# Performance work log

Hardware: AMD Instinct MI355X
Metric: run time of the kernel (lower is better)

Reference implementation:

```python
import jax, jax.numpy as jnp
import numpy as np
import math

B, DK, DV, T, H, W = 4, 64, 512, 2, 64, 64


def setup_inputs() -> dict:
    key = jax.random.key(0)
    k1, k2, k3, k4 = jax.random.split(key, 4)
    qkey = jax.random.normal(k1, (B, DK, H, W), dtype=jnp.float32)
    qval = jax.random.normal(k2, (B, DV, H, W), dtype=jnp.float32)
    mkey = jax.random.normal(k3, (B, DK, T, H, W), dtype=jnp.float32)
    mval = jax.random.normal(k4, (B, DV, T, H, W), dtype=jnp.float32)
    qmask = jnp.ones((B, 1, H, W), dtype=bool)
    mmask = jnp.ones((B, 1, T, H, W), dtype=bool)
    return {"qkey": qkey, "qval": qval, "qmask": qmask,
            "mkey": mkey, "mval": mval, "mmask": mmask}


def reference(qkey, qval, qmask, mkey, mval, mmask):
    # maskRead: masked cross-attention from query pixels to memory pixels.
    b, dk, h, w = qkey.shape
    dv = qval.shape[1]
    t = mkey.shape[2]
    n = h * w            # query positions
    m = t * h * w        # memory positions
    qk = qkey.reshape(b, dk, n)
    mk = mkey.reshape(b, dk, m)
    mv = mval.reshape(b, dv, m)
    qm = qmask.reshape(b, n)
    mm = mmask.reshape(b, m)
    scale = np.float32(1.0 / math.sqrt(dk))
    # scores[b, m, n] = mk^T @ qk  (softmax over memory axis m, as in torch dim=0)
    scores = jnp.einsum('bdm,bdn->bmn', mk, qk) * scale
    neg = jnp.asarray(-1e30, scores.dtype)
    scores = jnp.where(mm[:, :, None], scores, neg)
    p = jax.nn.softmax(scores, axis=1)  # [b, m, n]
    read = jnp.einsum('bvm,bmn->bvn', mv, p)  # [b, dv, n]
    # write only at masked query positions; elsewhere qread stays zero
    qread = jnp.where(qm[:, None, :], read, jnp.zeros_like(read))
    return qread.reshape(b, dv, h, w)
```

## Files before the change

### kernel.cpp

```cpp
#include <hip/hip_runtime.h>
#include <hip/hip_bf16.h>


#define NB 4
#define DKC 64
#define DVC 512
#define NQ 4096
#define NKV 8192
#define KB 64
#define NT2 128
#define DVG 128
#define NWG 512

typedef float f32x4 __attribute__((ext_vector_type(4)));
typedef float f32x16 __attribute__((ext_vector_type(16)));
typedef short s16x8 __attribute__((ext_vector_type(8)));
typedef unsigned short u16;
typedef unsigned int u32;
typedef u32 u32x4 __attribute__((ext_vector_type(4)));
typedef u16 u16x8 __attribute__((ext_vector_type(8)));
typedef u16 u16x4 __attribute__((ext_vector_type(4)));

__device__ __forceinline__ u16 f2bf_rne(float f) {
  union { float f; unsigned u; } v; v.f = f;
  return (u16)((v.u + 0x7FFFu + ((v.u >> 16) & 1u)) >> 16);
}

template <int SWZ>
__global__ __launch_bounds__(256) void transpose_bf16_64(
    const float* __restrict__ src, u16* __restrict__ dst, int M, float scale) {
  __shared__ float tt[64][65];
  const int tid = threadIdx.x;
  const int b = blockIdx.y;
  const int m0 = blockIdx.x * 64;
  {
    const int mi = tid & 63;
    const int dr = (tid >> 6) * 16;
    const float* s = src + ((size_t)b * 64 + dr) * M + m0 + mi;
#pragma unroll
    for (int j = 0; j < 16; ++j) tt[dr + j][mi] = s[(size_t)j * M];
  }
  __syncthreads();
  {
    const int mo = tid >> 2;
    const int d0 = (tid & 3) * 16;
    const int X = SWZ ? ((mo & 7) << 3) : 0;
    u16x8 o0, o1;
#pragma unroll
    for (int j = 0; j < 8; ++j) {
      o0[j] = f2bf_rne(tt[d0 + j][mo] * scale);
      o1[j] = f2bf_rne(tt[d0 + 8 + j][mo] * scale);
    }
    u16* base = dst + (size_t)b * M * 64 + (size_t)blockIdx.x * 4096 + mo * 64;
    *(u16x8*)(base + (d0 ^ X)) = o0;
    *(u16x8*)(base + ((d0 + 8) ^ X)) = o1;
  }
}

__global__ __launch_bounds__(256) void conv_v_tiles(const float* __restrict__ src,
                                                    u16* __restrict__ dst) {
  const size_t i = ((size_t)blockIdx.x * 256 + threadIdx.x) * 8;
  const int m = (int)(i & (NKV - 1));
  const size_t bd = i >> 13;
  const int dv = (int)(bd & (DVC - 1));
  const int b = (int)(bd >> 9);
  const float4 a = *(const float4*)(src + i);
  const float4 c = *(const float4*)(src + i + 4);
  u16x8 o;
  o[0] = f2bf_rne(a.x); o[1] = f2bf_rne(a.y); o[2] = f2bf_rne(a.z); o[3] = f2bf_rne(a.w);
  o[4] = f2bf_rne(c.x); o[5] = f2bf_rne(c.y); o[6] = f2bf_rne(c.z); o[7] = f2bf_rne(c.w);
  const int combo = b * 4 + (dv >> 7);
  const int row = dv & 127;
  const size_t off = (size_t)combo * (128 * 128 * 64) + (size_t)(m >> 6) * (128 * 64) +
                     row * 64 + ((m & 63) ^ ((row & 7) << 3));
  *(u16x8*)(dst + off) = o;
}

#define GLL(GP, LP)                                                            \
  __builtin_amdgcn_global_load_lds(                                            \
      (const __attribute__((address_space(1))) void*)(GP),                     \
      (__attribute__((address_space(3))) void*)(LP), 16, 0, 0)

#define PACK_QUARTER(SV, H, DST)                                               \
  {                                                                            \
    const float e0 = exp2f((SV)[(H) * 8 + 0]), e1 = exp2f((SV)[(H) * 8 + 1]);  \
    const float e2 = exp2f((SV)[(H) * 8 + 2]), e3 = exp2f((SV)[(H) * 8 + 3]);  \
    const float e4 = exp2f((SV)[(H) * 8 + 4]), e5 = exp2f((SV)[(H) * 8 + 5]);  \
    const float e6 = exp2f((SV)[(H) * 8 + 6]), e7 = exp2f((SV)[(H) * 8 + 7]);  \
    lacc += ((e0 + e1) + (e2 + e3)) + ((e4 + e5) + (e6 + e7));                 \
    u32 a0_, a1_, a2_, a3_;                                                    \
    asm("v_cvt_pk_bf16_f32 %0, %1, %2" : "=v"(a0_) : "v"(e0), "v"(e1));        \
    asm("v_cvt_pk_bf16_f32 %0, %1, %2" : "=v"(a1_) : "v"(e2), "v"(e3));        \
    asm("v_cvt_pk_bf16_f32 %0, %1, %2" : "=v"(a2_) : "v"(e4), "v"(e5));        \
    asm("v_cvt_pk_bf16_f32 %0, %1, %2" : "=v"(a3_) : "v"(e6), "v"(e7));        \
    asm("v_permlane32_swap_b32 %0, %1" : "+v"(a0_), "+v"(a2_));                \
    asm("v_permlane32_swap_b32 %0, %1" : "+v"(a1_), "+v"(a3_));                \
    union { u32x4 u; s16x8 s; } cv_;                                           \
    cv_.u[0] = a0_; cv_.u[1] = a1_; cv_.u[2] = a2_; cv_.u[3] = a3_;            \
    (DST) = cv_.s;                                                             \
  }

__global__ __launch_bounds__(256, 2) void maskread_main(
    const u16* __restrict__ kT, const u16* __restrict__ qT,
    const u16* __restrict__ vb, float* __restrict__ outp) {
  __shared__ __align__(16) u16 Vlds[2][DVG * KB];

  const int tid = threadIdx.x;
  const int w = tid >> 6;
  const int lane = tid & 63;
  const int l31 = lane & 31;
  const int hi = lane >> 5;

  const int logical = (blockIdx.x & 7) * (NWG / 8) + (blockIdx.x >> 3);
  const int combo = logical >> 5;
  const int qt = logical & 31;
  const int b = combo >> 2;
  const int g = combo & 3;
  const int nq = qt * 128 + w * 32 + l31;

  const u16* qp = qT + ((size_t)b * NQ + nq) * DKC + hi * 8;
  s16x8 qf[4];
#pragma unroll
  for (int ks = 0; ks < 4; ++ks) qf[ks] = *(const s16x8*)(qp + ks * 16);

  const int sw8 = (l31 & 7) << 3;
  int roff[4];
#pragma unroll
  for (int ks = 0; ks < 4; ++ks) roff[ks] = l31 * 64 + ((ks * 16 + hi * 8) ^ sw8);

  const u16* kgb = kT + (size_t)b * (128 * 4096);
  const u16* vgb = vb + (size_t)combo * (128 * 8192);

  f32x16 oacc[4];
#pragma unroll
  for (int dvt = 0; dvt < 4; ++dvt)
#pragma unroll
    for (int rr = 0; rr < 16; ++rr) oacc[dvt][rr] = 0.f;
  float lacc = 0.f;

  s16x8 ka[2][4];
#pragma unroll
  for (int kvt = 0; kvt < 2; ++kvt)
#pragma unroll
    for (int ks = 0; ks < 4; ++ks)
      ka[kvt][ks] = *(const s16x8*)(kgb + kvt * 2048 + roff[ks]);
  {
    const u16* vp0 = vgb + w * 2048 + lane * 8;
#pragma unroll
    for (int j = 0; j < 4; ++j) GLL(vp0 + j * 512, &Vlds[0][w * 2048 + j * 512]);
  }
  __syncthreads();

  for (int t = 0; t < NT2; ++t) {
    const int cur = t & 1;
    if (t + 1 < NT2) {
      const u16* vp_ = vgb + (size_t)(t + 1) * 8192 + w * 2048 + lane * 8;
#pragma unroll
      for (int j = 0; j < 4; ++j) GLL(vp_ + j * 512, &Vlds[cur ^ 1][w * 2048 + j * 512]);
    }

    f32x16 sacc[2];
#pragma unroll
    for (int kvt = 0; kvt < 2; ++kvt) {
#pragma unroll
      for (int rr = 0; rr < 16; ++rr) sacc[kvt][rr] = 0.f;
#pragma unroll
      for (int ks = 0; ks < 4; ++ks)
        sacc[kvt] = __builtin_amdgcn_mfma_f32_32x32x16_bf16(ka[kvt][ks], qf[ks], sacc[kvt], 0, 0, 0);
    }

    if (t + 1 < NT2) {
      const u16* kp_ = kgb + (size_t)(t + 1) * 4096;
#pragma unroll
      for (int kvt = 0; kvt < 2; ++kvt)
#pragma unroll
        for (int ks = 0; ks < 4; ++ks)
          ka[kvt][ks] = *(const s16x8*)(kp_ + kvt * 2048 + roff[ks]);
    }

    const u16* Vl = &Vlds[cur][0];
    __builtin_amdgcn_s_setprio(1);
    s16x8 pf[4];
#pragma unroll
    for (int ks = 0; ks < 4; ++ks) {
      PACK_QUARTER(sacc[ks >> 1], ks & 1, pf[ks]);
#pragma unroll
      for (int dvt = 0; dvt < 4; ++dvt) {
        const s16x8 va = *(const s16x8*)&Vl[roff[ks] + dvt * 2048];
        oacc[dvt] = __builtin_amdgcn_mfma_f32_32x32x16_bf16(va, pf[ks], oacc[dvt], 0, 0, 0);
      }
    }
    __builtin_amdgcn_s_setprio(0);

    __syncthreads();
  }

  const float lt = lacc + __shfl_xor(lacc, 32);
  const float rinv = 1.f / lt;
  float* ob = outp + ((size_t)(b * DVC + g * DVG)) * NQ + nq;
#pragma unroll
  for (int dvt = 0; dvt < 4; ++dvt)
#pragma unroll
    for (int rr = 0; rr < 16; ++rr) {
      const int dv = dvt * 32 + (rr & 3) + 8 * (rr >> 2) + 4 * hi;
      ob[(size_t)dv * NQ] = oacc[dvt][rr] * rinv;
    }
}

__global__ __launch_bounds__(512, 2) void maskread_attn_fb(
    const float* __restrict__ qkey, const float* __restrict__ mkey,
    const float* __restrict__ mval, float* __restrict__ out) {
  __shared__ __align__(16) u16 Qlds[64 * DKC];
  __shared__ __align__(16) u16 Klds1[128 * DKC];
  __shared__ __align__(16) u16 Plds1[64 * 128];
  __shared__ float psum_lds[8][64];

  const int tid = threadIdx.x;
  const int w = tid >> 6;
  const int l15 = tid & 15;
  const int lhi = (tid & 63) >> 4;
  const int logical = (blockIdx.x & 7) * 32 + (blockIdx.x >> 3);
  const int b = logical >> 6;
  const int n0 = (logical & 63) * 64;
  const float C2 = 0.18033688011112042f;

  {
    const int d = tid >> 3;
    const int q8 = (tid & 7) * 8;
    const float* src = qkey + ((b * DKC + d) * NQ) + n0 + q8;
    const float4 v0 = *(const float4*)(src);
    const float4 v1 = *(const float4*)(src + 4);
    const float vv[8] = {v0.x, v0.y, v0.z, v0.w, v1.x, v1.y, v1.z, v1.w};
#pragma unroll
    for (int j = 0; j < 8; ++j) {
      const int q = q8 + j;
      Qlds[q * DKC + (d ^ ((q & 7) << 3))] = f2bf_rne(vv[j]);
    }
  }

  f32x4 oacc[4][4];
#pragma unroll
  for (int mt = 0; mt < 4; ++mt)
#pragma unroll
    for (int nt = 0; nt < 4; ++nt)
#pragma unroll
      for (int i = 0; i < 4; ++i) oacc[mt][nt][i] = 0.f;
  float lacc[4] = {0.f, 0.f, 0.f, 0.f};

  const int dvb = w * 64;
  for (int kt = 0; kt < 64; ++kt) {
    const int kv0 = kt * 128;
    {
      const int d = tid >> 3;
      const int k16 = (tid & 7) * 16;
      const float* src = mkey + ((b * DKC + d) * NKV) + kv0 + k16;
#pragma unroll
      for (int i = 0; i < 4; ++i) {
        const float4 v = *(const float4*)(src + i * 4);
        const float vv4[4] = {v.x * C2, v.y * C2, v.z * C2, v.w * C2};
#pragma unroll
        for (int j = 0; j < 4; ++j) {
          const int k = k16 + i * 4 + j;
          Klds1[k * DKC + (d ^ ((k & 7) << 3))] = f2bf_rne(vv4[j]);
        }
      }
    }
    __syncthreads();
    f32x4 sacc[4];
#pragma unroll
    for (int nt = 0; nt < 4; ++nt)
#pragma unroll
      for (int i = 0; i < 4; ++i) sacc[nt][i] = 0.f;
#pragma unroll
    for (int ks = 0; ks < 2; ++ks) {
      const int kr = w * 16 + l15;
      const int c = ks * 32 + lhi * 8;
      const s16x8 afr = *(const s16x8*)&Klds1[kr * DKC + (c ^ ((kr & 7) << 3))];
#pragma unroll
      for (int nt = 0; nt < 4; ++nt) {
        const int q = nt * 16 + l15;
        const s16x8 bfr = *(const s16x8*)&Qlds[q * DKC + (c ^ ((q & 7) << 3))];
        sacc[nt] = __builtin_amdgcn_mfma_f32_16x16x32_bf16(afr, bfr, sacc[nt], 0, 0, 0);
      }
    }
#pragma unroll
    for (int nt = 0; nt < 4; ++nt) {
      const int q = nt * 16 + l15;
      const float p0 = exp2f(sacc[nt][0]);
      const float p1 = exp2f(sacc[nt][1]);
      const float p2 = exp2f(sacc[nt][2]);
      const float p3 = exp2f(sacc[nt][3]);
      lacc[nt] += (p0 + p1) + (p2 + p3);
      u16x4 pk;
      pk[0] = f2bf_rne(p0); pk[1] = f2bf_rne(p1); pk[2] = f2bf_rne(p2); pk[3] = f2bf_rne(p3);
      const int kvb = w * 16 + lhi * 4;
      *(u16x4*)&Plds1[q * 128 + (kvb ^ ((q & 7) << 3))] = pk;
    }
    __syncthreads();
#pragma unroll
    for (int ks = 0; ks < 4; ++ks) {
      s16x8 bfr[4];
#pragma unroll
      for (int nt = 0; nt < 4; ++nt) {
        const int q = nt * 16 + l15;
        const int kvb = ks * 32 + lhi * 8;
        bfr[nt] = *(const s16x8*)&Plds1[q * 128 + (kvb ^ ((q & 7) << 3))];
      }
#pragma unroll
      for (int mt = 0; mt < 4; ++mt) {
        const int vv = dvb + mt * 16 + l15;
        const float* src = mval + ((size_t)(b * DVC + vv) * NKV) + kv0 + ks * 32 + lhi * 8;
        const float4 a0 = *(const float4*)src;
        const float4 a1 = *(const float4*)(src + 4);
        s16x8 afr;
        afr[0] = (short)f2bf_rne(a0.x); afr[1] = (short)f2bf_rne(a0.y);
        afr[2] = (short)f2bf_rne(a0.z); afr[3] = (short)f2bf_rne(a0.w);
        afr[4] = (short)f2bf_rne(a1.x); afr[5] = (short)f2bf_rne(a1.y);
        afr[6] = (short)f2bf_rne(a1.z); afr[7] = (short)f2bf_rne(a1.w);
#pragma unroll
        for (int nt = 0; nt < 4; ++nt)
          oacc[mt][nt] = __builtin_amdgcn_mfma_f32_16x16x32_bf16(afr, bfr[nt], oacc[mt][nt], 0, 0, 0);
      }
    }
    __syncthreads();
  }
#pragma unroll
  for (int nt = 0; nt < 4; ++nt) {
    float l = lacc[nt];
    l += __shfl_xor(l, 16);
    l += __shfl_xor(l, 32);
    if (lhi == 0) psum_lds[w][nt * 16 + l15] = l;
  }
  __syncthreads();
  float linv[4];
#pragma unroll
  for (int nt = 0; nt < 4; ++nt) {
    const int q = nt * 16 + l15;
    float s = psum_lds[0][q];
#pragma unroll
    for (int ww = 1; ww < 8; ++ww) s += psum_lds[ww][q];
    linv[nt] = 1.f / s;
  }
#pragma unroll
  for (int mt = 0; mt < 4; ++mt) {
#pragma unroll
    for (int nt = 0; nt < 4; ++nt) {
      const int q = nt * 16 + l15;
#pragma unroll
      for (int i = 0; i < 4; ++i) {
        const int vv = dvb + mt * 16 + lhi * 4 + i;
        out[((size_t)(b * DVC + vv) * NQ) + n0 + q] = oacc[mt][nt][i] * linv[nt];
      }
    }
  }
}

extern "C" void kernel_launch(void* const* d_in, const int* in_sizes, int n_in,
                              void* d_out, int out_size, void* d_ws, size_t ws_size,
                              hipStream_t stream) {
  (void)in_sizes; (void)n_in; (void)out_size;
  const float* qkey = (const float*)d_in[0];
  const float* mkey = (const float*)d_in[3];
  const float* mval = (const float*)d_in[4];
  float* out = (float*)d_out;

  u16* kTp = (u16*)d_ws;
  u16* qTp = kTp + (size_t)NB * NKV * DKC;
  u16* vbp = qTp + (size_t)NB * NQ * DKC;
  const size_t need_base =
      ((size_t)NB * NKV * DKC + (size_t)NB * NQ * DKC + (size_t)NB * DVC * NKV) * 2;
  const float C2 = 0.18033688011112042f;

  if (ws_size >= need_base) {
    transpose_bf16_64<1><<<dim3(NKV / 64, NB), 256, 0, stream>>>(mkey, kTp, NKV, C2);
    transpose_bf16_64<0><<<dim3(NQ / 64, NB), 256, 0, stream>>>(qkey, qTp, NQ, 1.0f);
    conv_v_tiles<<<dim3((NB * DVC * NKV) / (256 * 8)), 256, 0, stream>>>(mval, vbp);
    maskread_main<<<dim3(NWG), dim3(256), 0, stream>>>(kTp, qTp, vbp, out);
  } else {
    maskread_attn_fb<<<dim3(256), dim3(512), 0, stream>>>(qkey, mkey, mval, out);
  }
}
```

Before: 281.7 us.

## Split KV loop across two wave groups per block with LDS reduction

Result: slower. 1.096 ms (+288.9%).

```diff
diff --git a/kernel.cpp b/kernel.cpp
--- a/kernel.cpp
+++ b/kernel.cpp
@@ -8,7 +8,6 @@
 #define NQ 4096
 #define NKV 8192
 #define KB 64
-#define NT2 128
 #define DVG 128
 #define NWG 512
 
@@ -100,23 +99,26 @@
     (DST) = cv_.s;                                                             \
   }
 
-__global__ __launch_bounds__(256, 2) void maskread_main(
+__global__ __launch_bounds__(512, 4) void maskread_main(
     const u16* __restrict__ kT, const u16* __restrict__ qT,
     const u16* __restrict__ vb, float* __restrict__ outp) {
-  __shared__ __align__(16) u16 Vlds[2][DVG * KB];
+  __shared__ __align__(16) unsigned char smem[69632];
 
   const int tid = threadIdx.x;
-  const int w = tid >> 6;
+  const int w4 = tid >> 6;
+  const int r = w4 >> 2;
+  const int wq = w4 & 3;
   const int lane = tid & 63;
   const int l31 = lane & 31;
   const int hi = lane >> 5;
+  const int t255 = tid & 255;
 
   const int logical = (blockIdx.x & 7) * (NWG / 8) + (blockIdx.x >> 3);
   const int combo = logical >> 5;
   const int qt = logical & 31;
   const int b = combo >> 2;
   const int g = combo & 3;
-  const int nq = qt * 128 + w * 32 + l31;
+  const int nq = qt * 128 + wq * 32 + l31;
 
   const u16* qp = qT + ((size_t)b * NQ + nq) * DKC + hi * 8;
   s16x8 qf[4];
@@ -128,8 +130,9 @@
 #pragma unroll
   for (int ks = 0; ks < 4; ++ks) roff[ks] = l31 * 64 + ((ks * 16 + hi * 8) ^ sw8);
 
-  const u16* kgb = kT + (size_t)b * (128 * 4096);
-  const u16* vgb = vb + (size_t)combo * (128 * 8192);
+  const u16* kgb = kT + (size_t)b * (128 * 4096) + (size_t)r * 64 * 4096;
+  const u16* vgb = vb + (size_t)combo * (128 * 8192) + (size_t)r * 64 * 8192;
+  u16* Vbase = (u16*)smem + r * 16384;
 
   f32x16 oacc[4];
 #pragma unroll
@@ -145,18 +148,19 @@
     for (int ks = 0; ks < 4; ++ks)
       ka[kvt][ks] = *(const s16x8*)(kgb + kvt * 2048 + roff[ks]);
   {
-    const u16* vp0 = vgb + w * 2048 + lane * 8;
-#pragma unroll
-    for (int j = 0; j < 4; ++j) GLL(vp0 + j * 512, &Vlds[0][w * 2048 + j * 512]);
+    const u16* vp0 = vgb + wq * 2048 + lane * 8;
+#pragma unroll
+    for (int j = 0; j < 4; ++j) GLL(vp0 + j * 512, Vbase + wq * 2048 + j * 512);
   }
   __syncthreads();
 
-  for (int t = 0; t < NT2; ++t) {
+  for (int t = 0; t < 64; ++t) {
     const int cur = t & 1;
-    if (t + 1 < NT2) {
-      const u16* vp_ = vgb + (size_t)(t + 1) * 8192 + w * 2048 + lane * 8;
-#pragma unroll
-      for (int j = 0; j < 4; ++j) GLL(vp_ + j * 512, &Vlds[cur ^ 1][w * 2048 + j * 512]);
+    if (t + 1 < 64) {
+      const u16* vp_ = vgb + (size_t)(t + 1) * 8192 + wq * 2048 + lane * 8;
+      u16* vd_ = Vbase + (cur ^ 1) * 8192 + wq * 2048;
+#pragma unroll
+      for (int j = 0; j < 4; ++j) GLL(vp_ + j * 512, vd_ + j * 512);
     }
 
     f32x16 sacc[2];
@@ -169,7 +173,7 @@
         sacc[kvt] = __builtin_amdgcn_mfma_f32_32x32x16_bf16(ka[kvt][ks], qf[ks], sacc[kvt], 0, 0, 0);
     }
 
-    if (t + 1 < NT2) {
+    if (t + 1 < 64) {
       const u16* kp_ = kgb + (size_t)(t + 1) * 4096;
 #pragma unroll
       for (int kvt = 0; kvt < 2; ++kvt)
@@ -178,16 +182,16 @@
           ka[kvt][ks] = *(const s16x8*)(kp_ + kvt * 2048 + roff[ks]);
     }
 
-    const u16* Vl = &Vlds[cur][0];
+    const u16* Vl = Vbase + cur * 8192;
     __builtin_amdgcn_s_setprio(1);
-    s16x8 pf[4];
 #pragma unroll
     for (int ks = 0; ks < 4; ++ks) {
-      PACK_QUARTER(sacc[ks >> 1], ks & 1, pf[ks]);
+      s16x8 pf;
+      PACK_QUARTER(sacc[ks >> 1], ks & 1, pf);
 #pragma unroll
       for (int dvt = 0; dvt < 4; ++dvt) {
         const s16x8 va = *(const s16x8*)&Vl[roff[ks] + dvt * 2048];
-        oacc[dvt] = __builtin_amdgcn_mfma_f32_32x32x16_bf16(va, pf[ks], oacc[dvt], 0, 0, 0);
+        oacc[dvt] = __builtin_amdgcn_mfma_f32_32x32x16_bf16(va, pf, oacc[dvt], 0, 0, 0);
       }
     }
     __builtin_amdgcn_s_setprio(0);
@@ -195,16 +199,44 @@
     __syncthreads();
   }
 
-  const float lt = lacc + __shfl_xor(lacc, 32);
+  const float ltr = lacc + __shfl_xor(lacc, 32);
+  float* redL = (float*)(smem + 67584);
+  redL[r * 256 + t255] = ltr;
+  float* X = (float*)smem;
+  if (r == 1) {
+#pragma unroll
+    for (int dvt = 0; dvt < 2; ++dvt)
+#pragma unroll
+      for (int rr = 0; rr < 16; ++rr) X[t255 * 33 + dvt * 16 + rr] = oacc[dvt][rr];
+  } else {
+#pragma unroll
+    for (int dvt = 0; dvt < 2; ++dvt)
+#pragma unroll
+      for (int rr = 0; rr < 16; ++rr) X[8448 + t255 * 33 + dvt * 16 + rr] = oacc[dvt + 2][rr];
+  }
+  __syncthreads();
+  const float lt = redL[t255] + redL[256 + t255];
   const float rinv = 1.f / lt;
   float* ob = outp + ((size_t)(b * DVC + g * DVG)) * NQ + nq;
-#pragma unroll
-  for (int dvt = 0; dvt < 4; ++dvt)
-#pragma unroll
-    for (int rr = 0; rr < 16; ++rr) {
-      const int dv = dvt * 32 + (rr & 3) + 8 * (rr >> 2) + 4 * hi;
-      ob[(size_t)dv * NQ] = oacc[dvt][rr] * rinv;
-    }
+  if (r == 0) {
+#pragma unroll
+    for (int dvt = 0; dvt < 2; ++dvt)
+#pragma unroll
+      for (int rr = 0; rr < 16; ++rr) {
+        const float v = oacc[dvt][rr] + X[t255 * 33 + dvt * 16 + rr];
+        const int dv = dvt * 32 + (rr & 3) + 8 * (rr >> 2) + 4 * hi;
+        ob[(size_t)dv * NQ] = v * rinv;
+      }
+  } else {
+#pragma unroll
+    for (int dvt = 0; dvt < 2; ++dvt)
+#pragma unroll
+      for (int rr = 0; rr < 16; ++rr) {
+        const float v = oacc[dvt + 2][rr] + X[8448 + t255 * 33 + dvt * 16 + rr];
+        const int dv = (dvt + 2) * 32 + (rr & 3) + 8 * (rr >> 2) + 4 * hi;
+        ob[(size_t)dv * NQ] = v * rinv;
+      }
+  }
 }
 
 __global__ __launch_bounds__(512, 2) void maskread_attn_fb(
@@ -375,7 +407,7 @@
     transpose_bf16_64<1><<<dim3(NKV / 64, NB), 256, 0, stream>>>(mkey, kTp, NKV, C2);
     transpose_bf16_64<0><<<dim3(NQ / 64, NB), 256, 0, stream>>>(qkey, qTp, NQ, 1.0f);
     conv_v_tiles<<<dim3((NB * DVC * NKV) / (256 * 8)), 256, 0, stream>>>(mval, vbp);
-    maskread_main<<<dim3(NWG), dim3(256), 0, stream>>>(kTp, qTp, vbp, out);
+    maskread_main<<<dim3(NWG), dim3(512), 0, stream>>>(kTp, qTp, vbp, out);
   } else {
     maskread_attn_fb<<<dim3(256), dim3(512), 0, stream>>>(qkey, mkey, mval, out);
   }
```
